# Performance work log

Hardware: AMD Instinct MI355X
Metric: run time of the kernel (lower is better)

The kernel has to match this reference:

```python
import jax, jax.numpy as jnp
import numpy as np

B, K, V, NB = 256, 62, 14522, 28

def setup_inputs() -> dict:
    key = jax.random.key(0)
    ks = jax.random.split(key, 10)
    thetas = jax.random.normal(ks[0], (B, K * 3), dtype=jnp.float32) * 0.2
    bone_lengths_core = jax.random.normal(ks[1], (B, NB), dtype=jnp.float32)
    center_bone_length = jax.random.uniform(ks[2], (B, 1), dtype=jnp.float32) + 0.5
    trans = jax.random.normal(ks[3], (B, 3), dtype=jnp.float32)
    scale = jax.random.uniform(ks[4], (B,), dtype=jnp.float32) + 0.5
    v_template = jax.random.normal(ks[5], (V, 3), dtype=jnp.float32) * 0.05
    t_pose_joints = jax.random.normal(ks[6], (K, 3), dtype=jnp.float32) * 0.1
    weights = jax.nn.softmax(jax.random.normal(ks[7], (V, K), dtype=jnp.float32) * 2.0, axis=1)
    # kinematic tree: parent[i] < i (binary-ish tree), parent[0] unused
    parents = jnp.maximum((jnp.arange(K) - 1) // 2, 0).astype(jnp.int64)
    bone_length_mapper = jax.random.randint(ks[8], (K,), -1, NB).astype(jnp.int64)
    return {"thetas": thetas, "bone_lengths_core": bone_lengths_core,
            "center_bone_length": center_bone_length, "trans": trans, "scale": scale,
            "v_template": v_template, "t_pose_joints": t_pose_joints, "weights": weights,
            "parents": parents, "bone_length_mapper": bone_length_mapper}

def euler2mat(r):
    # r: [N,3] ZYX euler angles -> [N,3,3]
    z, y, x = r[:, 0], r[:, 1], r[:, 2]
    cx, sx = jnp.cos(x), jnp.sin(x)
    cy, sy = jnp.cos(y), jnp.sin(y)
    cz, sz = jnp.cos(z), jnp.sin(z)
    one = jnp.ones_like(x)
    zero = jnp.zeros_like(x)
    Rx = jnp.stack([one, zero, zero, zero, cx, -sx, zero, sx, cx], -1).reshape(-1, 3, 3)
    Ry = jnp.stack([cy, zero, sy, zero, one, zero, -sy, zero, cy], -1).reshape(-1, 3, 3)
    Rz = jnp.stack([cz, -sz, zero, sz, cz, zero, zero, zero, one], -1).reshape(-1, 3, 3)
    return jnp.einsum('nij,njk,nkl->nil', Rz, Ry, Rx)

def _forward(thetas, bone_lengths_core, center_bone_length, trans, scale,
             v_template, t_pose_joints, weights, parents, bone_length_mapper):
    b = thetas.shape[0]
    k = t_pose_joints.shape[0]
    blc = jax.nn.sigmoid(bone_lengths_core / 5.0) * 2.0          # [B,28]
    R = euler2mat(thetas.reshape(-1, 3)).reshape(b, k, 3, 3)      # [B,K,3,3]
    Jt = t_pose_joints                                            # [K,3]
    # per-joint bone-length scale factor [B,K]
    gathered = blc[:, jnp.clip(bone_length_mapper, 0)]            # [B,K]
    factor = jnp.where(bone_length_mapper[None, :] < 0, 1.0, gathered)
    factor = factor.at[:, 1].set(center_bone_length[:, 0])
    factor = factor.at[:, 0].set(1.0)
    # local translations: root uses J0, others scaled offsets to parent
    off = (Jt - Jt[parents])[None] * factor[:, :, None]           # [B,K,3]
    off = off.at[:, 0].set(Jt[0][None])
    # local affines A [B,K,4,4]
    A = jnp.zeros((b, k, 4, 4), dtype=thetas.dtype)
    A = A.at[:, :, :3, :3].set(R)
    A = A.at[:, :, :3, 3].set(off)
    A = A.at[:, :, 3, 3].set(1.0)
    # compose along the kinematic tree
    G0 = jnp.zeros_like(A).at[:, 0].set(A[:, 0])
    def step(G_all, i):
        Gp = jnp.take(G_all, parents[i], axis=1)                  # [B,4,4]
        Gi = Gp @ jnp.take(A, i, axis=1)
        return jax.lax.dynamic_update_index_in_dim(G_all, Gi, i, axis=1), None
    G_all, _ = jax.lax.scan(step, G0, jnp.arange(1, k))
    J_final = G_all[:, :, :3, 3]                                  # [B,K,3]
    # subtract inverse-bind contribution: G' = G - pack(G @ [J;0])
    RJ = jnp.einsum('bkij,kj->bki', G_all[:, :, :3, :3], Jt)
    G = G_all.at[:, :, :3, 3].add(-RJ)
    # LBS skinning: T [B,V,4,4]
    T = jnp.einsum('bkij,vk->bvij', G, weights)
    rest_h = jnp.concatenate([v_template, jnp.ones((v_template.shape[0], 1), v_template.dtype)], axis=1)
    v = jnp.einsum('bvij,vj->bvi', T, rest_h)[:, :, :3]
    V_final = v * scale[:, None, None] + trans[:, None, :]
    J_out = J_final * scale[:, None, None] + trans[:, None, :]
    return V_final, J_out

def reference(thetas, bone_lengths_core, center_bone_length, trans, scale,
              v_template, t_pose_joints, weights, parents, bone_length_mapper):
    return _forward(thetas, bone_lengths_core, center_bone_length, trans, scale,
                    v_template, t_pose_joints, weights, parents, bone_length_mapper)
```

## Files before the change

kernel.cpp:

```cpp
#include <hip/hip_runtime.h>

#define NJ     62
#define NV     14522
#define NCORE  28
#define KPAD   256
#define OUTF   (NV * 3)
#define MT32   454
#define EREG   100

typedef __attribute__((ext_vector_type(8))) short short8v;
typedef __attribute__((ext_vector_type(4))) short short4v;
typedef __attribute__((ext_vector_type(4))) float floatx4;
typedef __attribute__((ext_vector_type(2))) float floatx2;

#define AS1(p) ((const __attribute__((address_space(1))) void*)(p))
#define AS3(p) ((__attribute__((address_space(3))) void*)(p))

#define SCHED0() __builtin_amdgcn_sched_barrier(0)
#define WAITVM0() do { SCHED0(); asm volatile("s_waitcnt vmcnt(0)" ::: "memory"); SCHED0(); } while (0)

static __device__ inline short f2bf(float x) {
    unsigned u = __float_as_uint(x);
    unsigned r = (u + 0x7fffu + ((u >> 16) & 1u)) >> 16;
    return (short)r;
}

static __device__ inline short8v pack8(float a0, float a1, float a2, float a3,
                                       float a4, float a5, float a6, float a7) {
    union { unsigned u[4]; short8v v; } p;
    asm("v_cvt_pk_bf16_f32 %0, %1, %2" : "=v"(p.u[0]) : "v"(a0), "v"(a1));
    asm("v_cvt_pk_bf16_f32 %0, %1, %2" : "=v"(p.u[1]) : "v"(a2), "v"(a3));
    asm("v_cvt_pk_bf16_f32 %0, %1, %2" : "=v"(p.u[2]) : "v"(a4), "v"(a5));
    asm("v_cvt_pk_bf16_f32 %0, %1, %2" : "=v"(p.u[3]) : "v"(a6), "v"(a7));
    return p.v;
}

static __device__ inline unsigned swz(unsigned off) {
    return off ^ (((off >> 9) & 7u) << 4);
}

__global__ __launch_bounds__(256) void fk_kernel(
    const float* __restrict__ thetas, const float* __restrict__ blc,
    const float* __restrict__ cbl, const float* __restrict__ trans,
    const float* __restrict__ scale, const float* __restrict__ tpose,
    const int* __restrict__ parents, const int* __restrict__ mapper,
    short* __restrict__ Bt, float* __restrict__ Jout)
{
    __shared__ float Asm[4][NJ][12];
    __shared__ float Gsm[4][NJ][12];

    const int w = threadIdx.x >> 6;
    const int b = blockIdx.x * 4 + w;
    const int k = threadIdx.x & 63;
    int p = 0;

    if (k < NJ) {
        p = parents[k];
        const float tz = thetas[(b * NJ + k) * 3 + 0];
        const float ty = thetas[(b * NJ + k) * 3 + 1];
        const float tx = thetas[(b * NJ + k) * 3 + 2];
        const float cx = cosf(tx), sx = sinf(tx);
        const float cy = cosf(ty), sy = sinf(ty);
        const float cz = cosf(tz), sz = sinf(tz);
        const float r00 = cz * cy;
        const float r01 = cz * sy * sx - sz * cx;
        const float r02 = sz * sx + cz * sy * cx;
        const float r10 = sz * cy;
        const float r11 = cz * cx + sz * sy * sx;
        const float r12 = sz * sy * cx - cz * sx;
        const float r20 = -sy;
        const float r21 = cy * sx;
        const float r22 = cy * cx;

        float f;
        const int m = mapper[k];
        if (k == 0)        f = 1.0f;
        else if (k == 1)   f = cbl[b];
        else if (m < 0)    f = 1.0f;
        else               f = 2.0f / (1.0f + expf(-blc[b * NCORE + m] * 0.2f));

        float ox, oy, oz;
        if (k == 0) {
            ox = tpose[0]; oy = tpose[1]; oz = tpose[2];
        } else {
            ox = (tpose[k * 3 + 0] - tpose[p * 3 + 0]) * f;
            oy = (tpose[k * 3 + 1] - tpose[p * 3 + 1]) * f;
            oz = (tpose[k * 3 + 2] - tpose[p * 3 + 2]) * f;
        }
        Asm[w][k][0] = r00; Asm[w][k][1] = r01; Asm[w][k][2]  = r02; Asm[w][k][3]  = ox;
        Asm[w][k][4] = r10; Asm[w][k][5] = r11; Asm[w][k][6]  = r12; Asm[w][k][7]  = oy;
        Asm[w][k][8] = r20; Asm[w][k][9] = r21; Asm[w][k][10] = r22; Asm[w][k][11] = oz;
    }
    __syncthreads();

    if (k == 0) {
        #pragma unroll
        for (int j = 0; j < 12; ++j) Gsm[w][0][j] = Asm[w][0][j];
    }
    __syncthreads();

    const int depth = (k < NJ) ? (31 - __clz((unsigned)(k + 1))) : 99;
    for (int d = 1; d <= 5; ++d) {
        if (depth == d) {
            float gp[12], a[12], g[12];
            #pragma unroll
            for (int j = 0; j < 12; ++j) { gp[j] = Gsm[w][p][j]; a[j] = Asm[w][k][j]; }
            #pragma unroll
            for (int i = 0; i < 3; ++i) {
                #pragma unroll
                for (int j = 0; j < 4; ++j) {
                    float s = (j == 3) ? gp[i * 4 + 3] : 0.0f;
                    s = fmaf(gp[i * 4 + 0], a[0 * 4 + j], s);
                    s = fmaf(gp[i * 4 + 1], a[1 * 4 + j], s);
                    s = fmaf(gp[i * 4 + 2], a[2 * 4 + j], s);
                    g[i * 4 + j] = s;
                }
            }
            #pragma unroll
            for (int j = 0; j < 12; ++j) Gsm[w][k][j] = g[j];
        }
        __syncthreads();
    }

    if (k < NJ) {
        float g[12];
        #pragma unroll
        for (int j = 0; j < 12; ++j) g[j] = Gsm[w][k][j];
        const float jx = tpose[k * 3 + 0];
        const float jy = tpose[k * 3 + 1];
        const float jz = tpose[k * 3 + 2];
        const float s  = scale[b];
        Jout[(b * NJ + k) * 3 + 0] = fmaf(g[3],  s, trans[b * 3 + 0]);
        Jout[(b * NJ + k) * 3 + 1] = fmaf(g[7],  s, trans[b * 3 + 1]);
        Jout[(b * NJ + k) * 3 + 2] = fmaf(g[11], s, trans[b * 3 + 2]);
        float np[3];
        np[0] = g[3]  - (g[0] * jx + g[1] * jy + g[2]  * jz);
        np[1] = g[7]  - (g[4] * jx + g[5] * jy + g[6]  * jz);
        np[2] = g[11] - (g[8] * jx + g[9] * jy + g[10] * jz);
        #pragma unroll
        for (int i = 0; i < 3; ++i) {
            short4v o;
            o[0] = f2bf(g[i * 4 + 0]);
            o[1] = f2bf(g[i * 4 + 1]);
            o[2] = f2bf(g[i * 4 + 2]);
            o[3] = f2bf(np[i]);
            *(short4v*)&Bt[(size_t)(b * 3 + i) * KPAD + k * 4] = o;
        }
        if (k == 0) {
            short4v z = {0, 0, 0, 0};
            #pragma unroll
            for (int i = 0; i < 3; ++i) {
                *(short4v*)&Bt[(size_t)(b * 3 + i) * KPAD + 248] = z;
                *(short4v*)&Bt[(size_t)(b * 3 + i) * KPAD + 252] = z;
            }
        }
    }
}

__global__ __launch_bounds__(256, 3) void gemm_skin(
    const float* __restrict__ W,
    const float* __restrict__ vt,
    const short* __restrict__ Bt,
    const float* __restrict__ scale,
    const float* __restrict__ trans,
    float* __restrict__ out)
{
    __shared__ __align__(16) char ldsB[48 * 512];
    __shared__ __align__(16) float epi_all[4 * 16 * EREG];

    const int tid  = threadIdx.x;
    const int wave = tid >> 6;
    const int lane = tid & 63;
    const int lrow = lane & 15;
    const int lk   = lane >> 4;
    const int yy    = blockIdx.x / 48;
    const int inner = blockIdx.x - yy * 48;
    const int s     = inner * 4 + wave;
    const int start  = (s < 70) ? s * 3 : 210 + (s - 70) * 2;
    const int ntiles = (s < 70) ? 3 : 2;
    const int b0 = yy * 16;
    float* epi = epi_all + wave * 16 * EREG;

    {
        const char* Bsrc = (const char*)(Bt + (size_t)yy * 48 * KPAD);
        #pragma unroll
        for (int cc = 0; cc < 6; ++cc) {
            const unsigned Lb = (unsigned)(wave * 6144 + cc * 1024);
            __builtin_amdgcn_global_load_lds(AS1(Bsrc + swz(Lb + lane * 16)),
                                             AS3(ldsB + Lb), 16, 0, 0);
        }
    }

    float sv[3], tv[3]; int bl3[3], ii3[3];
    #pragma unroll
    for (int nt = 0; nt < 3; ++nt) {
        const int n_loc = nt * 16 + lrow;
        bl3[nt] = n_loc / 3; ii3[nt] = n_loc - bl3[nt] * 3;
        sv[nt] = scale[b0 + bl3[nt]];
        tv[nt] = trans[(b0 + bl3[nt]) * 3 + ii3[nt]];
    }
    unsigned bofs[3], bxor[3];
    #pragma unroll
    for (int nt = 0; nt < 3; ++nt) {
        const unsigned brow = nt * 16 + lrow;
        bofs[nt] = brow * 512;
        bxor[nt] = (brow & 7u) << 4;
    }

    WAITVM0();
    __syncthreads();

    for (int t = 0; t < ntiles; ++t) {
        const int mt32 = start + t;
        int vr0 = mt32 * 32 + lrow;      if (vr0 > NV - 1) vr0 = NV - 1;
        int vr1 = mt32 * 32 + 16 + lrow; if (vr1 > NV - 1) vr1 = NV - 1;

        const float* Wr0 = W + (size_t)vr0 * NJ;
        const float* Wr1 = W + (size_t)vr1 * NJ;
        floatx2 wc0[8], wc1[8];
        #pragma unroll
        for (int k8 = 0; k8 < 8; ++k8) {
            const int j0 = k8 * 8 + lk * 2;
            wc0[k8] = (j0 < NJ) ? *(const floatx2*)(Wr0 + j0) : (floatx2){0.f, 0.f};
            wc1[k8] = (j0 < NJ) ? *(const floatx2*)(Wr1 + j0) : (floatx2){0.f, 0.f};
        }
        const float h0x = vt[vr0 * 3 + 0], h0y = vt[vr0 * 3 + 1], h0z = vt[vr0 * 3 + 2];
        const float h1x = vt[vr1 * 3 + 0], h1y = vt[vr1 * 3 + 1], h1z = vt[vr1 * 3 + 2];

        floatx4 acc0[3], acc1[3];
        #pragma unroll
        for (int nt = 0; nt < 3; ++nt) {
            acc0[nt] = (floatx4){0.f, 0.f, 0.f, 0.f};
            acc1[nt] = (floatx4){0.f, 0.f, 0.f, 0.f};
        }
        #pragma unroll
        for (int k8 = 0; k8 < 8; ++k8) {
            const float w00 = wc0[k8][0], w01 = wc0[k8][1];
            const float w10 = wc1[k8][0], w11 = wc1[k8][1];
            const short8v a0 = pack8(w00 * h0x, w00 * h0y, w00 * h0z, w00,
                                     w01 * h0x, w01 * h0y, w01 * h0z, w01);
            const short8v a1 = pack8(w10 * h1x, w10 * h1y, w10 * h1z, w10,
                                     w11 * h1x, w11 * h1y, w11 * h1z, w11);
            const unsigned cb = (unsigned)(k8 * 4 + lk) * 16;
            #pragma unroll
            for (int nt = 0; nt < 3; ++nt) {
                const short8v bf = *(const short8v*)(ldsB + bofs[nt] + (cb ^ bxor[nt]));
                acc0[nt] = __builtin_amdgcn_mfma_f32_16x16x32_bf16(a0, bf, acc0[nt], 0, 0, 0);
                acc1[nt] = __builtin_amdgcn_mfma_f32_16x16x32_bf16(a1, bf, acc1[nt], 0, 0, 0);
            }
        }

        #pragma unroll
        for (int nt = 0; nt < 3; ++nt) {
            #pragma unroll
            for (int r = 0; r < 4; ++r) {
                const int m0 = (lk * 4 + r) * 3;
                epi[bl3[nt] * EREG + m0 + ii3[nt]] =
                    fmaf(acc0[nt][r], sv[nt], tv[nt]);
                epi[bl3[nt] * EREG + 48 + m0 + ii3[nt]] =
                    fmaf(acc1[nt][r], sv[nt], tv[nt]);
            }
        }

        const int m96 = mt32 * 96;
        const bool edge = (m96 + 96 > OUTF);
        #pragma unroll
        for (int it = 0; it < 12; ++it) {
            const int idx = it * 64 + lane;
            const int r = idx / 48, j = idx - r * 48;
            const floatx2 val = *(const floatx2*)&epi[r * EREG + 2 * j];
            const int pp = m96 + 2 * j;
            if (!edge || pp + 1 < OUTF)
                *(floatx2*)&out[(size_t)(b0 + r) * OUTF + pp] = val;
        }
    }
}

extern "C" void kernel_launch(void* const* d_in, const int* in_sizes, int n_in,
                              void* d_out, int out_size, void* d_ws, size_t ws_size,
                              hipStream_t stream)
{
    const float* thetas  = (const float*)d_in[0];
    const float* blc     = (const float*)d_in[1];
    const float* cbl     = (const float*)d_in[2];
    const float* trans   = (const float*)d_in[3];
    const float* scale   = (const float*)d_in[4];
    const float* vtempl  = (const float*)d_in[5];
    const float* tpose   = (const float*)d_in[6];
    const float* weights = (const float*)d_in[7];
    const int*   parents = (const int*)d_in[8];
    const int*   mapper  = (const int*)d_in[9];

    float* out  = (float*)d_out;
    float* Jout = out + (size_t)256 * NV * 3;

    short* Bt = (short*)d_ws;

    fk_kernel<<<64, 256, 0, stream>>>(thetas, blc, cbl, trans, scale, tpose,
                                      parents, mapper, Bt, Jout);
    gemm_skin<<<768, 256, 0, stream>>>(weights, vtempl, Bt, scale, trans, out);
}
```

Measured before the change: 28.35 us.

## Prefetch next tile's skin weights with contiguous vector loads and permute B layout

The GEMM skinning loop now loads each lane's 16 contiguous weight floats as four float4 loads, and it prefetches the next tile's weights and vertex template into registers while the current tile's MFMAs run. To match the new contiguous K assignment per lane (lk*16), the producer kernel writes the bf16 bone-transform rows in a permuted K order. The last padding column is zeroed explicitly because the float4 read runs past joint 61 into the next row. The aim is to hide global load latency and cut load instruction count, at the cost of more live registers and an overread past the end of W on the final row.

```diff
diff --git a/kernel.cpp b/kernel.cpp
--- a/kernel.cpp
+++ b/kernel.cpp
@@ -137,6 +137,10 @@
         np[0] = g[3]  - (g[0] * jx + g[1] * jy + g[2]  * jz);
         np[1] = g[7]  - (g[4] * jx + g[5] * jy + g[6]  * jz);
         np[2] = g[11] - (g[8] * jx + g[9] * jy + g[10] * jz);
+
+        const int lkj = k >> 4;
+        const int rr  = k & 15;
+        const int qb  = 32 * (rr >> 1) + 8 * lkj + 4 * (rr & 1);
         #pragma unroll
         for (int i = 0; i < 3; ++i) {
             short4v o;
@@ -144,7 +148,7 @@
             o[1] = f2bf(g[i * 4 + 1]);
             o[2] = f2bf(g[i * 4 + 2]);
             o[3] = f2bf(np[i]);
-            *(short4v*)&Bt[(size_t)(b * 3 + i) * KPAD + k * 4] = o;
+            *(short4v*)&Bt[(size_t)(b * 3 + i) * KPAD + qb] = o;
         }
         if (k == 0) {
             short4v z = {0, 0, 0, 0};
@@ -191,13 +195,14 @@
         }
     }
 
-    float sv[3], tv[3]; int bl3[3], ii3[3];
+    float sv[3], tv[3]; int eoff[3];
     #pragma unroll
     for (int nt = 0; nt < 3; ++nt) {
         const int n_loc = nt * 16 + lrow;
-        bl3[nt] = n_loc / 3; ii3[nt] = n_loc - bl3[nt] * 3;
-        sv[nt] = scale[b0 + bl3[nt]];
-        tv[nt] = trans[(b0 + bl3[nt]) * 3 + ii3[nt]];
+        const int bl = n_loc / 3, ii = n_loc - bl * 3;
+        eoff[nt] = bl * EREG + ii;
+        sv[nt] = scale[b0 + bl];
+        tv[nt] = trans[(b0 + bl) * 3 + ii];
     }
     unsigned bofs[3], bxor[3];
     #pragma unroll
@@ -207,25 +212,46 @@
         bxor[nt] = (brow & 7u) << 4;
     }
 
+    floatx4 wc0[4], wc1[4]; float h0x, h0y, h0z, h1x, h1y, h1z;
+    {
+        int vr0 = start * 32 + lrow;      if (vr0 > NV - 1) vr0 = NV - 1;
+        int vr1 = start * 32 + 16 + lrow; if (vr1 > NV - 1) vr1 = NV - 1;
+        const float* Wb0 = W + (size_t)vr0 * NJ + lk * 16;
+        const float* Wb1 = W + (size_t)vr1 * NJ + lk * 16;
+        #pragma unroll
+        for (int c = 0; c < 4; ++c) {
+            wc0[c] = *(const floatx4*)(Wb0 + 4 * c);
+            wc1[c] = *(const floatx4*)(Wb1 + 4 * c);
+        }
+        h0x = vt[vr0 * 3 + 0]; h0y = vt[vr0 * 3 + 1]; h0z = vt[vr0 * 3 + 2];
+        h1x = vt[vr1 * 3 + 0]; h1y = vt[vr1 * 3 + 1]; h1z = vt[vr1 * 3 + 2];
+    }
+
     WAITVM0();
     __syncthreads();
 
     for (int t = 0; t < ntiles; ++t) {
-        const int mt32 = start + t;
-        int vr0 = mt32 * 32 + lrow;      if (vr0 > NV - 1) vr0 = NV - 1;
-        int vr1 = mt32 * 32 + 16 + lrow; if (vr1 > NV - 1) vr1 = NV - 1;
-
-        const float* Wr0 = W + (size_t)vr0 * NJ;
-        const float* Wr1 = W + (size_t)vr1 * NJ;
-        floatx2 wc0[8], wc1[8];
-        #pragma unroll
-        for (int k8 = 0; k8 < 8; ++k8) {
-            const int j0 = k8 * 8 + lk * 2;
-            wc0[k8] = (j0 < NJ) ? *(const floatx2*)(Wr0 + j0) : (floatx2){0.f, 0.f};
-            wc1[k8] = (j0 < NJ) ? *(const floatx2*)(Wr1 + j0) : (floatx2){0.f, 0.f};
-        }
-        const float h0x = vt[vr0 * 3 + 0], h0y = vt[vr0 * 3 + 1], h0z = vt[vr0 * 3 + 2];
-        const float h1x = vt[vr1 * 3 + 0], h1y = vt[vr1 * 3 + 1], h1z = vt[vr1 * 3 + 2];
+        floatx4 wn0[4], wn1[4];
+        float g0x = 0.f, g0y = 0.f, g0z = 0.f, g1x = 0.f, g1y = 0.f, g1z = 0.f;
+        if (t + 1 < ntiles) {
+            int vr0 = (start + t + 1) * 32 + lrow;      if (vr0 > NV - 1) vr0 = NV - 1;
+            int vr1 = (start + t + 1) * 32 + 16 + lrow; if (vr1 > NV - 1) vr1 = NV - 1;
+            const float* Wb0 = W + (size_t)vr0 * NJ + lk * 16;
+            const float* Wb1 = W + (size_t)vr1 * NJ + lk * 16;
+            #pragma unroll
+            for (int c = 0; c < 4; ++c) {
+                wn0[c] = *(const floatx4*)(Wb0 + 4 * c);
+                wn1[c] = *(const floatx4*)(Wb1 + 4 * c);
+            }
+            g0x = vt[vr0 * 3 + 0]; g0y = vt[vr0 * 3 + 1]; g0z = vt[vr0 * 3 + 2];
+            g1x = vt[vr1 * 3 + 0]; g1y = vt[vr1 * 3 + 1]; g1z = vt[vr1 * 3 + 2];
+        } else {
+            #pragma unroll
+            for (int c = 0; c < 4; ++c) {
+                wn0[c] = (floatx4){0.f, 0.f, 0.f, 0.f};
+                wn1[c] = (floatx4){0.f, 0.f, 0.f, 0.f};
+            }
+        }
 
         floatx4 acc0[3], acc1[3];
         #pragma unroll
@@ -235,8 +261,11 @@
         }
         #pragma unroll
         for (int k8 = 0; k8 < 8; ++k8) {
-            const float w00 = wc0[k8][0], w01 = wc0[k8][1];
-            const float w10 = wc1[k8][0], w11 = wc1[k8][1];
+            float w00 = wc0[k8 >> 1][2 * (k8 & 1)];
+            float w01 = wc0[k8 >> 1][2 * (k8 & 1) + 1];
+            float w10 = wc1[k8 >> 1][2 * (k8 & 1)];
+            float w11 = wc1[k8 >> 1][2 * (k8 & 1) + 1];
+            if (lk == 3 && k8 == 7) { w00 = w01 = w10 = w11 = 0.f; }
             const short8v a0 = pack8(w00 * h0x, w00 * h0y, w00 * h0z, w00,
                                      w01 * h0x, w01 * h0y, w01 * h0z, w01);
             const short8v a1 = pack8(w10 * h1x, w10 * h1y, w10 * h1z, w10,
@@ -255,14 +284,12 @@
             #pragma unroll
             for (int r = 0; r < 4; ++r) {
                 const int m0 = (lk * 4 + r) * 3;
-                epi[bl3[nt] * EREG + m0 + ii3[nt]] =
-                    fmaf(acc0[nt][r], sv[nt], tv[nt]);
-                epi[bl3[nt] * EREG + 48 + m0 + ii3[nt]] =
-                    fmaf(acc1[nt][r], sv[nt], tv[nt]);
-            }
-        }
-
-        const int m96 = mt32 * 96;
+                epi[eoff[nt] + m0]      = fmaf(acc0[nt][r], sv[nt], tv[nt]);
+                epi[eoff[nt] + 48 + m0] = fmaf(acc1[nt][r], sv[nt], tv[nt]);
+            }
+        }
+
+        const int m96 = (start + t) * 96;
         const bool edge = (m96 + 96 > OUTF);
         #pragma unroll
         for (int it = 0; it < 12; ++it) {
@@ -273,6 +300,11 @@
             if (!edge || pp + 1 < OUTF)
                 *(floatx2*)&out[(size_t)(b0 + r) * OUTF + pp] = val;
         }
+
+        #pragma unroll
+        for (int c = 0; c < 4; ++c) { wc0[c] = wn0[c]; wc1[c] = wn1[c]; }
+        h0x = g0x; h0y = g0y; h0z = g0z;
+        h1x = g1x; h1y = g1y; h1z = g1z;
     }
 }
 
```

Measured after the change: 28.56 us. Within noise of the previous version (+0.7%).
